# Kernel tuning notes

Hardware: AMD Instinct MI355X
Metric: run time of the kernel (lower is better)

Reference implementation:

```python
import jax, jax.numpy as jnp
import numpy as np

WS = (4, 4, 4)          # window size (d, h, w)
NUM_HEADS = 6
DIM = 192


def _relative_position_index(ws):
    # static int index, computed in numpy
    coords = np.stack(np.meshgrid(np.arange(ws[0]), np.arange(ws[1]), np.arange(ws[2]), indexing='ij'))  # (3, wd, wh, ww)
    coords = coords.reshape(3, -1)                      # (3, N)
    rel = coords[:, :, None] - coords[:, None, :]        # (3, N, N)
    rel = rel.transpose(1, 2, 0)                         # (N, N, 3)
    rel[:, :, 0] += ws[0] - 1
    rel[:, :, 1] += ws[1] - 1
    rel[:, :, 2] += ws[2] - 1
    rel[:, :, 0] *= (2 * ws[1] - 1) * (2 * ws[2] - 1)
    rel[:, :, 1] *= (2 * ws[2] - 1)
    return rel.sum(-1)                                   # (N, N)

_REL_IDX = _relative_position_index(WS)


def setup_inputs() -> dict:
    key = jax.random.key(0)
    ks = jax.random.split(key, 4)
    x = jax.random.normal(ks[0], (2, DIM, 46, 47, 48), dtype=jnp.float32)
    qkv_w = jax.random.normal(ks[1], (3 * DIM, DIM), dtype=jnp.float32) * 0.02
    qkv_b = jnp.zeros((3 * DIM,), dtype=jnp.float32)
    proj_w = jax.random.normal(ks[2], (DIM, DIM), dtype=jnp.float32) * 0.02
    proj_b = jnp.zeros((DIM,), dtype=jnp.float32)
    rpb_table = jax.random.normal(ks[3], ((2 * WS[0] - 1) * (2 * WS[1] - 1) * (2 * WS[2] - 1), NUM_HEADS), dtype=jnp.float32) * 0.02
    return {"x": x, "qkv_w": qkv_w, "qkv_b": qkv_b, "proj_w": proj_w, "proj_b": proj_b, "rpb_table": rpb_table}


def reference(x, qkv_w, qkv_b, proj_w, proj_b, rpb_table):
    B, C, D, H, W = x.shape
    wd, wh, ww = WS
    pd = (-D) % wd
    ph = (-H) % wh
    pw = (-W) % ww
    Dp, Hp, Wp = D + pd, H + ph, W + pw

    # BCDHW -> B,D,H,W,C then pad spatial dims (zero pad, same as F.pad on BCDHW)
    xc = jnp.transpose(x, (0, 2, 3, 4, 1))
    xc = jnp.pad(xc, ((0, 0), (0, pd), (0, ph), (0, pw), (0, 0)))

    # window partition -> (nW, N, C)
    Dw, Hw, Ww = Dp // wd, Hp // wh, Wp // ww
    xw = xc.reshape(B, Dw, wd, Hw, wh, Ww, ww, C)
    xw = jnp.transpose(xw, (0, 1, 3, 5, 2, 4, 6, 7)).reshape(-1, wd * wh * ww, C)
    N = wd * wh * ww

    # windowed MHA with relative position bias
    hd = C // NUM_HEADS
    qkv = xw @ qkv_w.T + qkv_b                               # (nW, N, 3C)
    qkv = qkv.reshape(-1, N, 3, NUM_HEADS, hd)
    q, k, v = (jnp.transpose(qkv[:, :, i], (0, 2, 1, 3)) for i in range(3))  # (nW, h, N, hd)
    scale = jnp.asarray(hd, x.dtype) ** -0.5
    attn = jnp.einsum('whnd,whmd->whnm', q * scale, k)       # (nW, h, N, N)
    bias = rpb_table[_REL_IDX.reshape(-1)].reshape(N, N, NUM_HEADS)
    bias = jnp.transpose(bias, (2, 0, 1))                    # (h, N, N)
    attn = jax.nn.softmax(attn + bias[None], axis=-1)
    out = jnp.einsum('whnm,whmd->whnd', attn, v)             # (nW, h, N, hd)
    out = jnp.transpose(out, (0, 2, 1, 3)).reshape(-1, N, C)
    out = out @ proj_w.T + proj_b

    # window reverse + crop, back to BCDHW
    xr = out.reshape(B, Dw, Hw, Ww, wd, wh, ww, C)
    xr = jnp.transpose(xr, (0, 1, 4, 2, 5, 3, 6, 7)).reshape(B, Dp, Hp, Wp, C)
    xr = jnp.transpose(xr, (0, 4, 1, 2, 3))[:, :, :D, :H, :W]
    return xr
```

## Files before the change

kernel.cpp:

```cpp
#include <hip/hip_runtime.h>

typedef __bf16 bf16x8 __attribute__((ext_vector_type(8)));
typedef __bf16 bf16x4 __attribute__((ext_vector_type(4)));
typedef float  f32x4  __attribute__((ext_vector_type(4)));

#define MFMA16(a, b, c) __builtin_amdgcn_mfma_f32_16x16x32_bf16((a), (b), (c), 0, 0, 0)

constexpr int Cdim = 192, NHd = 6;
constexpr int Dd = 46, Hh = 47, Wl = 48;
constexpr int HWst = Hh * Wl;
constexpr int NWIN_PER_B = 12 * 12 * 12;
constexpr int NBLK = 2 * NWIN_PER_B;
constexpr float SCALE = 0.17677669529663687f;

constexpr int WQ_ELEMS = 576 * 192;
constexpr int WP_ELEMS = 192 * 192;
constexpr size_t OFF_WQ   = 0;
constexpr size_t OFF_WP   = OFF_WQ + WQ_ELEMS;
constexpr size_t OFF_RPBT = OFF_WP + WP_ELEMS;
constexpr size_t WS_SMALL = (OFF_RPBT + 4128) * 2;

__device__ inline bf16x8 cvt8(const float* __restrict__ p) {
  f32x4 u0 = *(const f32x4*)p;
  f32x4 u1 = *(const f32x4*)(p + 4);
  bf16x8 r;
  r[0] = (__bf16)u0[0]; r[1] = (__bf16)u0[1]; r[2] = (__bf16)u0[2]; r[3] = (__bf16)u0[3];
  r[4] = (__bf16)u1[0]; r[5] = (__bf16)u1[1]; r[6] = (__bf16)u1[2]; r[7] = (__bf16)u1[3];
  return r;
}

__device__ inline bf16x4 pack4(f32x4 v) {
  bf16x4 r;
  r[0] = (__bf16)v[0]; r[1] = (__bf16)v[1]; r[2] = (__bf16)v[2]; r[3] = (__bf16)v[3];
  return r;
}

__device__ inline bf16x8 cat8(bf16x4 a, bf16x4 b) {
  bf16x8 r;
  r[0] = a[0]; r[1] = a[1]; r[2] = a[2]; r[3] = a[3];
  r[4] = b[0]; r[5] = b[1]; r[6] = b[2]; r[7] = b[3];
  return r;
}

__global__ __launch_bounds__(256) void convert_w_kernel(
    const float* __restrict__ qkv_w, const float* __restrict__ proj_w,
    const float* __restrict__ rpb,
    __bf16* __restrict__ wq, __bf16* __restrict__ wp, float* __restrict__ rpbt) {
  const int i = blockIdx.x * 256 + threadIdx.x;
  if (i < WQ_ELEMS) wq[i] = (__bf16)qkv_w[i];
  if (i < WP_ELEMS) wp[i] = (__bf16)proj_w[i];
  if (i < 343 * NHd) {
    const int h = i / 343, idx = i % 343;
    rpbt[h * 343 + idx] = rpb[idx * NHd + h];
  }
}

constexpr int XWA  = 204;
constexpr int QKLD = 36;
constexpr int VLD  = 68;
constexpr int BUFE = 2304;

__global__ __launch_bounds__(384, 4) void fused_kernel(
    const float* __restrict__ x, const float* __restrict__ qkv_b,
    const __bf16* __restrict__ wq, const __bf16* __restrict__ wp,
    const float* __restrict__ proj_b, const float* __restrict__ rpbt,
    float* __restrict__ out)
{
  __shared__ __bf16 xw[64 * XWA];
  __shared__ __bf16 bufs[6 * BUFE];
  const f32x4 fz = {0.f, 0.f, 0.f, 0.f};
  const int tid = threadIdx.x, lane = tid & 63, wv = tid >> 6;
  const int li = lane & 15, g = lane >> 4;
  const int hq = wv;
  const int bid = blockIdx.x;
  const int wid = (bid & 7) * (NBLK / 8) + (bid >> 3);
  const int b = wid / NWIN_PER_B, wr = wid % NWIN_PER_B;
  const int d0 = (wr / 144) * 4, h0 = ((wr / 12) % 12) * 4, w0 = (wr % 12) * 4;

  #pragma unroll
  for (int rep = 0; rep < 8; ++rep) {
    const int task = rep * 384 + tid;
    const int c = task % Cdim, ph = task / Cdim;
    const int dd = ph >> 2, hh = ph & 3;
    const int d = d0 + dd, hs = h0 + hh;
    f32x4 v = fz;
    if (d < Dd && hs < Hh)
      v = *(const f32x4*)(x + ((size_t)(b * Cdim + c) * Dd + d) * HWst + hs * Wl + w0);
    const int nb = (dd * 16 + hh * 4) * XWA + c;
    xw[nb]           = (__bf16)v[0];
    xw[nb + XWA]     = (__bf16)v[1];
    xw[nb + 2 * XWA] = (__bf16)v[2];
    xw[nb + 3 * XWA] = (__bf16)v[3];
  }
  __syncthreads();

  __bf16* buf = bufs + wv * BUFE;
  bf16x8 qfv[4], kfv[4], vav[2][2];

  {
    f32x4 acc[2][4];
    #pragma unroll
    for (int i = 0; i < 2; ++i)
      #pragma unroll
      for (int t = 0; t < 4; ++t) acc[i][t] = fz;
    #pragma unroll
    for (int kk = 0; kk < 6; ++kk) {
      const int k0 = kk * 32 + g * 8;
      bf16x8 xf[4];
      #pragma unroll
      for (int nt = 0; nt < 4; ++nt)
        xf[nt] = *(const bf16x8*)&xw[(nt * 16 + li) * XWA + k0];
      #pragma unroll
      for (int i = 0; i < 2; ++i) {
        bf16x8 wf = *(const bf16x8*)(wq + (size_t)((hq * 2 + i) * 16 + li) * Cdim + k0);
        #pragma unroll
        for (int nt = 0; nt < 4; ++nt)
          acc[i][nt] = MFMA16(wf, xf[nt], acc[i][nt]);
      }
    }
    #pragma unroll
    for (int i = 0; i < 2; ++i) {
      const f32x4 b4 = *(const f32x4*)(qkv_b + (hq * 2 + i) * 16 + g * 4);
      #pragma unroll
      for (int nt = 0; nt < 4; ++nt) {
        f32x4 val = (acc[i][nt] + b4) * SCALE;
        *(bf16x4*)&buf[(nt * 16 + li) * QKLD + i * 16 + g * 4] = pack4(val);
      }
    }
    #pragma unroll
    for (int t = 0; t < 4; ++t) {
      bf16x4 lo = *(const bf16x4*)&buf[(t * 16 + li) * QKLD + g * 8];
      bf16x4 hi = *(const bf16x4*)&buf[(t * 16 + li) * QKLD + g * 8 + 4];
      qfv[t] = cat8(lo, hi);
    }
  }

  {
    f32x4 acc[2][4];
    #pragma unroll
    for (int i = 0; i < 2; ++i)
      #pragma unroll
      for (int t = 0; t < 4; ++t) acc[i][t] = fz;
    #pragma unroll
    for (int kk = 0; kk < 6; ++kk) {
      const int k0 = kk * 32 + g * 8;
      bf16x8 xf[4];
      #pragma unroll
      for (int nt = 0; nt < 4; ++nt)
        xf[nt] = *(const bf16x8*)&xw[(nt * 16 + li) * XWA + k0];
      #pragma unroll
      for (int i = 0; i < 2; ++i) {
        bf16x8 wf = *(const bf16x8*)(wq + (size_t)(192 + (hq * 2 + i) * 16 + li) * Cdim + k0);
        #pragma unroll
        for (int nt = 0; nt < 4; ++nt)
          acc[i][nt] = MFMA16(wf, xf[nt], acc[i][nt]);
      }
    }
    #pragma unroll
    for (int i = 0; i < 2; ++i) {
      const f32x4 b4 = *(const f32x4*)(qkv_b + 192 + (hq * 2 + i) * 16 + g * 4);
      #pragma unroll
      for (int nt = 0; nt < 4; ++nt) {
        f32x4 val = acc[i][nt] + b4;
        *(bf16x4*)&buf[(nt * 16 + li) * QKLD + i * 16 + g * 4] = pack4(val);
      }
    }
    #pragma unroll
    for (int t = 0; t < 4; ++t) {
      bf16x4 lo = *(const bf16x4*)&buf[(t * 16 + li) * QKLD + g * 8];
      bf16x4 hi = *(const bf16x4*)&buf[(t * 16 + li) * QKLD + g * 8 + 4];
      kfv[t] = cat8(lo, hi);
    }
  }

  {
    f32x4 acc[2][4];
    #pragma unroll
    for (int i = 0; i < 2; ++i)
      #pragma unroll
      for (int t = 0; t < 4; ++t) acc[i][t] = fz;
    #pragma unroll
    for (int kk = 0; kk < 6; ++kk) {
      const int k0 = kk * 32 + g * 8;
      bf16x8 xf[4];
      #pragma unroll
      for (int rt = 0; rt < 4; ++rt)
        xf[rt] = *(const bf16x8*)&xw[(rt * 16 + li) * XWA + k0];
      #pragma unroll
      for (int i = 0; i < 2; ++i) {
        bf16x8 wf = *(const bf16x8*)(wq + (size_t)(384 + (hq * 2 + i) * 16 + li) * Cdim + k0);
        #pragma unroll
        for (int rt = 0; rt < 4; ++rt)
          acc[i][rt] = MFMA16(xf[rt], wf, acc[i][rt]);
      }
    }
    #pragma unroll
    for (int i = 0; i < 2; ++i) {
      const float bias = qkv_b[384 + (hq * 2 + i) * 16 + li];
      const f32x4 vb = {bias, bias, bias, bias};
      #pragma unroll
      for (int rt = 0; rt < 4; ++rt) {
        f32x4 val = acc[i][rt] + vb;
        *(bf16x4*)&buf[(i * 16 + li) * VLD + rt * 16 + g * 4] = pack4(val);
      }
    }
    #pragma unroll
    for (int rt = 0; rt < 2; ++rt)
      #pragma unroll
      for (int kk = 0; kk < 2; ++kk) {
        bf16x4 lo = *(const bf16x4*)&buf[(rt * 16 + li) * VLD + kk * 32 + g * 4];
        bf16x4 hi = *(const bf16x4*)&buf[(rt * 16 + li) * VLD + kk * 32 + 16 + g * 4];
        vav[rt][kk] = cat8(lo, hi);
      }
  }
  __syncthreads();

  __bf16* ao = xw;

  const int hbase = ((li >> 2) - g + 3) * 7 + (li & 3) + 3;
  float brow[7][4];
  {
    const float* rp = rpbt + hq * 343 + hbase - 3;
    #pragma unroll
    for (int dd = 0; dd < 7; ++dd)
      #pragma unroll
      for (int j = 0; j < 4; ++j)
        brow[dd][j] = rp[dd * 49 + j];
  }

  #pragma unroll
  for (int rb = 0; rb < 4; ++rb) {
    f32x4 s[4];
    #pragma unroll
    for (int ct = 0; ct < 4; ++ct) s[ct] = MFMA16(kfv[ct], qfv[rb], fz);

    float t[4][4];
    float rm = -3e38f;
    #pragma unroll
    for (int ct = 0; ct < 4; ++ct) {
      #pragma unroll
      for (int r = 0; r < 4; ++r) {
        const float tv = s[ct][r] + brow[rb - ct + 3][3 - r];
        t[ct][r] = tv;
        rm = fmaxf(rm, tv);
      }
    }
    rm = fmaxf(rm, __shfl_xor(rm, 16));
    rm = fmaxf(rm, __shfl_xor(rm, 32));
    float rs = 0.f;
    #pragma unroll
    for (int ct = 0; ct < 4; ++ct)
      #pragma unroll
      for (int r = 0; r < 4; ++r) {
        const float p = __expf(t[ct][r] - rm);
        t[ct][r] = p;
        rs += p;
      }
    rs += __shfl_xor(rs, 16);
    rs += __shfl_xor(rs, 32);
    const float rinv = 1.f / rs;

    bf16x4 ppk[4];
    #pragma unroll
    for (int ct = 0; ct < 4; ++ct) {
      f32x4 pv = {t[ct][0] * rinv, t[ct][1] * rinv, t[ct][2] * rinv, t[ct][3] * rinv};
      ppk[ct] = pack4(pv);
    }
    bf16x8 pa0 = cat8(ppk[0], ppk[1]);
    bf16x8 pa1 = cat8(ppk[2], ppk[3]);

    f32x4 o0 = fz, o1 = fz;
    o0 = MFMA16(vav[0][0], pa0, o0);
    o0 = MFMA16(vav[0][1], pa1, o0);
    o1 = MFMA16(vav[1][0], pa0, o1);
    o1 = MFMA16(vav[1][1], pa1, o1);
    *(bf16x4*)&ao[(rb * 16 + li) * XWA + hq * 32 + g * 4]      = pack4(o0);
    *(bf16x4*)&ao[(rb * 16 + li) * XWA + hq * 32 + 16 + g * 4] = pack4(o1);
  }
  __syncthreads();

  f32x4 pacc[2][4];
  #pragma unroll
  for (int i = 0; i < 2; ++i)
    #pragma unroll
    for (int rt = 0; rt < 4; ++rt) pacc[i][rt] = fz;
  #pragma unroll
  for (int kk = 0; kk < 6; ++kk) {
    const int k0 = kk * 32 + g * 8;
    bf16x8 af[4];
    #pragma unroll
    for (int rt = 0; rt < 4; ++rt)
      af[rt] = *(const bf16x8*)&ao[(rt * 16 + li) * XWA + k0];
    #pragma unroll
    for (int i = 0; i < 2; ++i) {
      const int c = (wv * 2 + i) * 16 + li;
      bf16x8 bf = *(const bf16x8*)(wp + (size_t)c * Cdim + k0);
      #pragma unroll
      for (int rt = 0; rt < 4; ++rt)
        pacc[i][rt] = MFMA16(af[rt], bf, pacc[i][rt]);
    }
  }
  #pragma unroll
  for (int i = 0; i < 2; ++i) {
    const int c = (wv * 2 + i) * 16 + li;
    const float pb = proj_b[c];
    #pragma unroll
    for (int rt = 0; rt < 4; ++rt) {
      const int d = d0 + rt, hs = h0 + g;
      if (d < Dd && hs < Hh) {
        f32x4 vv = {pacc[i][rt][0] + pb, pacc[i][rt][1] + pb,
                    pacc[i][rt][2] + pb, pacc[i][rt][3] + pb};
        *(f32x4*)(out + ((size_t)(b * Cdim + c) * Dd + d) * HWst + hs * Wl + w0) = vv;
      }
    }
  }
}

constexpr int XW_LD = 200, QK_LD = 36, VT_LD = 68, P_LDF = 68;
constexpr int XW_OFF  = 0;
constexpr int Q_OFF   = 25600;
constexpr int K_OFF   = Q_OFF + 27648;
constexpr int VT_OFF  = K_OFF + 27648;
constexpr int P_OFF   = VT_OFF + 26112;
constexpr int RPB_OFF = P_OFF + 26112;
constexpr int LDS_TOTAL = RPB_OFF + 8256;

__global__ __launch_bounds__(768, 3) void winattn_fused(
    const float* __restrict__ x, const float* __restrict__ qkv_w,
    const float* __restrict__ qkv_b, const float* __restrict__ proj_w,
    const float* __restrict__ proj_b, const float* __restrict__ rpb,
    float* __restrict__ out)
{
  extern __shared__ __align__(16) char smem[];
  __bf16* xw  = (__bf16*)(smem + XW_OFF);
  __bf16* qs  = (__bf16*)(smem + Q_OFF);
  __bf16* ks  = (__bf16*)(smem + K_OFF);
  __bf16* vt  = (__bf16*)(smem + VT_OFF);
  __bf16* pl  = (__bf16*)(smem + P_OFF);
  float*  rps = (float*)(smem + RPB_OFF);
  const f32x4 fz = {0.f, 0.f, 0.f, 0.f};
  const int tid = threadIdx.x, lane = tid & 63, wv = tid >> 6;
  const int hq = wv >> 1, half = wv & 1, li = lane & 15, g = lane >> 4;
  const int bid = blockIdx.x;
  const int wid = (bid & 7) * (NBLK / 8) + (bid >> 3);
  const int b = wid / NWIN_PER_B, wr = wid % NWIN_PER_B;
  const int d0 = (wr / 144) * 4, h0 = ((wr / 12) % 12) * 4, w0 = (wr % 12) * 4;
  for (int i = tid; i < 343 * NHd; i += 768) rps[i] = rpb[i];
  #pragma unroll
  for (int rep = 0; rep < 4; ++rep) {
    const int task = rep * 768 + tid;
    const int c = task % Cdim, ph = task / Cdim;
    const int dd = ph >> 2, hh2 = ph & 3;
    const int d = d0 + dd, hsp = h0 + hh2;
    f32x4 v = fz;
    if (d < Dd && hsp < Hh)
      v = *(const f32x4*)(x + ((size_t)(b * Cdim + c) * Dd + d) * HWst + hsp * Wl + w0);
    const int nb = (dd * 16 + hh2 * 4) * XW_LD + c;
    xw[nb] = (__bf16)v[0]; xw[nb + XW_LD] = (__bf16)v[1];
    xw[nb + 2 * XW_LD] = (__bf16)v[2]; xw[nb + 3 * XW_LD] = (__bf16)v[3];
  }
  __syncthreads();
  {
    f32x4 acc[6][2];
    #pragma unroll
    for (int it = 0; it < 6; ++it)
      #pragma unroll
      for (int rr = 0; rr < 2; ++rr) acc[it][rr] = fz;
    #pragma unroll
    for (int kk = 0; kk < 6; ++kk) {
      const int k0 = kk * 32 + g * 8;
      bf16x8 af[2];
      #pragma unroll
      for (int rr = 0; rr < 2; ++rr)
        af[rr] = *(const bf16x8*)&xw[((half * 2 + rr) * 16 + li) * XW_LD + k0];
      #pragma unroll
      for (int it = 0; it < 6; ++it) {
        const int T = (it >> 1) * 12 + hq * 2 + (it & 1);
        const int j = T * 16 + li;
        bf16x8 bf = cvt8(qkv_w + j * Cdim + k0);
        #pragma unroll
        for (int rr = 0; rr < 2; ++rr) acc[it][rr] = MFMA16(af[rr], bf, acc[it][rr]);
      }
    }
    #pragma unroll
    for (int it = 0; it < 6; ++it) {
      const int part = it >> 1, e16 = (it & 1) * 16;
      const int j0 = (part * 12 + hq * 2 + (it & 1)) * 16;
      const float qb = qkv_b[j0 + li];
      #pragma unroll
      for (int rr = 0; rr < 2; ++rr) {
        const int rb = half * 2 + rr;
        #pragma unroll
        for (int r = 0; r < 4; ++r) {
          const float val = acc[it][rr][r] + qb;
          const int n = rb * 16 + g * 4 + r;
          if (part == 0)      qs[(hq * 64 + n) * QK_LD + e16 + li] = (__bf16)val;
          else if (part == 1) ks[(hq * 64 + n) * QK_LD + e16 + li] = (__bf16)val;
          else                vt[(hq * 32 + e16 + li) * VT_LD + n] = (__bf16)val;
        }
      }
    }
  }
  __syncthreads();
  {
    __bf16* pw = pl + wv * 16 * P_LDF;
    #pragma unroll 1
    for (int rr = 0; rr < 2; ++rr) {
      const int rb = half * 2 + rr;
      bf16x8 aq = *(const bf16x8*)&qs[(hq * 64 + rb * 16 + li) * QK_LD + g * 8];
      f32x4 s[4];
      #pragma unroll
      for (int ct = 0; ct < 4; ++ct) {
        bf16x8 bk = *(const bf16x8*)&ks[(hq * 64 + ct * 16 + li) * QK_LD + g * 8];
        s[ct] = MFMA16(aq, bk, fz);
      }
      float t[4][4], rm[4] = {-3e38f, -3e38f, -3e38f, -3e38f};
      #pragma unroll
      for (int ct = 0; ct < 4; ++ct) {
        #pragma unroll
        for (int r = 0; r < 4; ++r) {
          const int idx = (rb - ct + 3) * 49 + (g - (li >> 2) + 3) * 7 + (r - (li & 3) + 3);
          const float tv = s[ct][r] * SCALE + rps[idx * NHd + hq];
          t[ct][r] = tv;
          rm[r] = fmaxf(rm[r], tv);
        }
      }
      #pragma unroll
      for (int r = 0; r < 4; ++r) {
        rm[r] = fmaxf(rm[r], __shfl_xor(rm[r], 1, 16));
        rm[r] = fmaxf(rm[r], __shfl_xor(rm[r], 2, 16));
        rm[r] = fmaxf(rm[r], __shfl_xor(rm[r], 4, 16));
        rm[r] = fmaxf(rm[r], __shfl_xor(rm[r], 8, 16));
      }
      float rs[4] = {0, 0, 0, 0};
      #pragma unroll
      for (int ct = 0; ct < 4; ++ct)
        #pragma unroll
        for (int r = 0; r < 4; ++r) {
          const float p = __expf(t[ct][r] - rm[r]);
          t[ct][r] = p; rs[r] += p;
        }
      #pragma unroll
      for (int r = 0; r < 4; ++r) {
        rs[r] += __shfl_xor(rs[r], 1, 16);
        rs[r] += __shfl_xor(rs[r], 2, 16);
        rs[r] += __shfl_xor(rs[r], 4, 16);
        rs[r] += __shfl_xor(rs[r], 8, 16);
      }
      #pragma unroll
      for (int ct = 0; ct < 4; ++ct)
        #pragma unroll
        for (int r = 0; r < 4; ++r)
          pw[(g * 4 + r) * P_LDF + ct * 16 + li] = (__bf16)t[ct][r];
      f32x4 o[2] = {fz, fz};
      #pragma unroll
      for (int kk = 0; kk < 2; ++kk) {
        bf16x8 ap = *(const bf16x8*)&pw[li * P_LDF + kk * 32 + g * 8];
        #pragma unroll
        for (int ct = 0; ct < 2; ++ct) {
          bf16x8 bv = *(const bf16x8*)&vt[(hq * 32 + ct * 16 + li) * VT_LD + kk * 32 + g * 8];
          o[ct] = MFMA16(ap, bv, o[ct]);
        }
      }
      float inv[4];
      #pragma unroll
      for (int r = 0; r < 4; ++r) inv[r] = 1.f / rs[r];
      #pragma unroll
      for (int ct = 0; ct < 2; ++ct)
        #pragma unroll
        for (int r = 0; r < 4; ++r)
          xw[(rb * 16 + g * 4 + r) * XW_LD + hq * 32 + ct * 16 + li] = (__bf16)(o[ct][r] * inv[r]);
    }
  }
  __syncthreads();
  {
    f32x4 acc[4];
    #pragma unroll
    for (int rt = 0; rt < 4; ++rt) acc[rt] = fz;
    const int c = wv * 16 + li;
    #pragma unroll
    for (int kk = 0; kk < 6; ++kk) {
      const int k0 = kk * 32 + g * 8;
      bf16x8 bf = cvt8(proj_w + c * Cdim + k0);
      #pragma unroll
      for (int rt = 0; rt < 4; ++rt) {
        bf16x8 af = *(const bf16x8*)&xw[(rt * 16 + li) * XW_LD + k0];
        acc[rt] = MFMA16(af, bf, acc[rt]);
      }
    }
    const float pb = proj_b[c];
    #pragma unroll
    for (int rt = 0; rt < 4; ++rt) {
      const int d = d0 + rt, hsp = h0 + g;
      if (d < Dd && hsp < Hh) {
        f32x4 vv = {acc[rt][0] + pb, acc[rt][1] + pb, acc[rt][2] + pb, acc[rt][3] + pb};
        *(f32x4*)(out + ((size_t)(b * Cdim + c) * Dd + d) * HWst + hsp * Wl + w0) = vv;
      }
    }
  }
}

extern "C" void kernel_launch(void* const* d_in, const int* in_sizes, int n_in,
                              void* d_out, int out_size, void* d_ws, size_t ws_size,
                              hipStream_t stream) {
  const float* x      = (const float*)d_in[0];
  const float* qkv_w  = (const float*)d_in[1];
  const float* qkv_b  = (const float*)d_in[2];
  const float* proj_w = (const float*)d_in[3];
  const float* proj_b = (const float*)d_in[4];
  const float* rpb    = (const float*)d_in[5];
  float* out = (float*)d_out;

  if (ws_size >= WS_SMALL) {
    __bf16* wsb  = (__bf16*)d_ws;
    __bf16* wq   = wsb + OFF_WQ;
    __bf16* wp   = wsb + OFF_WP;
    float*  rpbt = (float*)(wsb + OFF_RPBT);
    convert_w_kernel<<<(WQ_ELEMS + 255) / 256, 256, 0, stream>>>(qkv_w, proj_w, rpb, wq, wp, rpbt);
    fused_kernel<<<NBLK, 384, 0, stream>>>(x, qkv_b, wq, wp, proj_b, rpbt, out);
  } else {
    (void)hipFuncSetAttribute(reinterpret_cast<const void*>(&winattn_fused),
                              hipFuncAttributeMaxDynamicSharedMemorySize, LDS_TOTAL);
    winattn_fused<<<NBLK, 768, LDS_TOTAL, stream>>>(
        x, qkv_w, qkv_b, proj_w, proj_b, rpb, out);
  }
}
```

Baseline: 300.5 us.

## Process two adjacent windows per block with ping-pong LDS regions

Each block now handles two neighbouring windows along W instead of one, halving the grid. The relative-position bias rows are loaded once per block and reused for both windows. Two LDS regions swap roles, so the second window's input staging is issued right after the first window's projection, letting global loads overlap that epilogue. LDS per block grows (two 6*BUFE regions), which may reduce resident blocks per CU, and there is less block-level parallelism.

New measurement: 402.2 us. 1.34x slower.

```diff
diff --git a/kernel.cpp b/kernel.cpp
--- a/kernel.cpp
+++ b/kernel.cpp
@@ -11,6 +11,7 @@
 constexpr int HWst = Hh * Wl;
 constexpr int NWIN_PER_B = 12 * 12 * 12;
 constexpr int NBLK = 2 * NWIN_PER_B;
+constexpr int NPAIR = NBLK / 2;
 constexpr float SCALE = 0.17677669529663687f;
 
 constexpr int WQ_ELEMS = 576 * 192;
@@ -59,43 +60,40 @@
 constexpr int QKLD = 36;
 constexpr int VLD  = 68;
 constexpr int BUFE = 2304;
-
-__global__ __launch_bounds__(384, 4) void fused_kernel(
-    const float* __restrict__ x, const float* __restrict__ qkv_b,
-    const __bf16* __restrict__ wq, const __bf16* __restrict__ wp,
-    const float* __restrict__ proj_b, const float* __restrict__ rpbt,
-    float* __restrict__ out)
-{
-  __shared__ __bf16 xw[64 * XWA];
-  __shared__ __bf16 bufs[6 * BUFE];
+constexpr int REGE = 6 * BUFE;
+
+struct LaneCtx {
+  int tid, li, g, hq;
+  int b, d0, h0;
+};
+
+__device__ inline void stage_x(const float* __restrict__ x, __bf16* __restrict__ xw,
+                               const LaneCtx& L, int w0) {
   const f32x4 fz = {0.f, 0.f, 0.f, 0.f};
-  const int tid = threadIdx.x, lane = tid & 63, wv = tid >> 6;
-  const int li = lane & 15, g = lane >> 4;
-  const int hq = wv;
-  const int bid = blockIdx.x;
-  const int wid = (bid & 7) * (NBLK / 8) + (bid >> 3);
-  const int b = wid / NWIN_PER_B, wr = wid % NWIN_PER_B;
-  const int d0 = (wr / 144) * 4, h0 = ((wr / 12) % 12) * 4, w0 = (wr % 12) * 4;
-
   #pragma unroll
   for (int rep = 0; rep < 8; ++rep) {
-    const int task = rep * 384 + tid;
+    const int task = rep * 384 + L.tid;
     const int c = task % Cdim, ph = task / Cdim;
     const int dd = ph >> 2, hh = ph & 3;
-    const int d = d0 + dd, hs = h0 + hh;
+    const int d = L.d0 + dd, hs = L.h0 + hh;
     f32x4 v = fz;
     if (d < Dd && hs < Hh)
-      v = *(const f32x4*)(x + ((size_t)(b * Cdim + c) * Dd + d) * HWst + hs * Wl + w0);
+      v = *(const f32x4*)(x + ((size_t)(L.b * Cdim + c) * Dd + d) * HWst + hs * Wl + w0);
     const int nb = (dd * 16 + hh * 4) * XWA + c;
     xw[nb]           = (__bf16)v[0];
     xw[nb + XWA]     = (__bf16)v[1];
     xw[nb + 2 * XWA] = (__bf16)v[2];
     xw[nb + 3 * XWA] = (__bf16)v[3];
   }
-  __syncthreads();
-
-  __bf16* buf = bufs + wv * BUFE;
-  bf16x8 qfv[4], kfv[4], vav[2][2];
+}
+
+__device__ inline void gemm_qkv(const __bf16* __restrict__ xw, __bf16* __restrict__ bufreg,
+                                const float* __restrict__ qkv_b, const __bf16* __restrict__ wq,
+                                const LaneCtx& L,
+                                bf16x8 (&qfv)[4], bf16x8 (&kfv)[4], bf16x8 (&vav)[2][2]) {
+  const f32x4 fz = {0.f, 0.f, 0.f, 0.f};
+  const int li = L.li, g = L.g, hq = L.hq;
+  __bf16* buf = bufreg + hq * BUFE;
 
   {
     f32x4 acc[2][4];
@@ -134,7 +132,6 @@
       qfv[t] = cat8(lo, hi);
     }
   }
-
   {
     f32x4 acc[2][4];
     #pragma unroll
@@ -172,7 +169,6 @@
       kfv[t] = cat8(lo, hi);
     }
   }
-
   {
     f32x4 acc[2][4];
     #pragma unroll
@@ -213,21 +209,14 @@
         vav[rt][kk] = cat8(lo, hi);
       }
   }
-  __syncthreads();
-
-  __bf16* ao = xw;
-
-  const int hbase = ((li >> 2) - g + 3) * 7 + (li & 3) + 3;
-  float brow[7][4];
-  {
-    const float* rp = rpbt + hq * 343 + hbase - 3;
-    #pragma unroll
-    for (int dd = 0; dd < 7; ++dd)
-      #pragma unroll
-      for (int j = 0; j < 4; ++j)
-        brow[dd][j] = rp[dd * 49 + j];
-  }
-
+}
+
+__device__ inline void attn_phase(__bf16* __restrict__ ao, const LaneCtx& L,
+                                  const float (&brow)[7][4],
+                                  const bf16x8 (&qfv)[4], const bf16x8 (&kfv)[4],
+                                  const bf16x8 (&vav)[2][2]) {
+  const f32x4 fz = {0.f, 0.f, 0.f, 0.f};
+  const int li = L.li, g = L.g, hq = L.hq;
   #pragma unroll
   for (int rb = 0; rb < 4; ++rb) {
     f32x4 s[4];
@@ -277,8 +266,13 @@
     *(bf16x4*)&ao[(rb * 16 + li) * XWA + hq * 32 + g * 4]      = pack4(o0);
     *(bf16x4*)&ao[(rb * 16 + li) * XWA + hq * 32 + 16 + g * 4] = pack4(o1);
   }
-  __syncthreads();
-
+}
+
+__device__ inline void proj_phase(const __bf16* __restrict__ ao, const __bf16* __restrict__ wp,
+                                  const float* __restrict__ proj_b, const LaneCtx& L,
+                                  int w0, float* __restrict__ out) {
+  const f32x4 fz = {0.f, 0.f, 0.f, 0.f};
+  const int li = L.li, g = L.g, wv = L.hq;
   f32x4 pacc[2][4];
   #pragma unroll
   for (int i = 0; i < 2; ++i)
@@ -306,14 +300,64 @@
     const float pb = proj_b[c];
     #pragma unroll
     for (int rt = 0; rt < 4; ++rt) {
-      const int d = d0 + rt, hs = h0 + g;
+      const int d = L.d0 + rt, hs = L.h0 + g;
       if (d < Dd && hs < Hh) {
         f32x4 vv = {pacc[i][rt][0] + pb, pacc[i][rt][1] + pb,
                     pacc[i][rt][2] + pb, pacc[i][rt][3] + pb};
-        *(f32x4*)(out + ((size_t)(b * Cdim + c) * Dd + d) * HWst + hs * Wl + w0) = vv;
-      }
-    }
-  }
+        *(f32x4*)(out + ((size_t)(L.b * Cdim + c) * Dd + d) * HWst + hs * Wl + w0) = vv;
+      }
+    }
+  }
+}
+
+__global__ __launch_bounds__(384, 4) void fused_kernel(
+    const float* __restrict__ x, const float* __restrict__ qkv_b,
+    const __bf16* __restrict__ wq, const __bf16* __restrict__ wp,
+    const float* __restrict__ proj_b, const float* __restrict__ rpbt,
+    float* __restrict__ out)
+{
+  __shared__ __bf16 regA[REGE];
+  __shared__ __bf16 regB[REGE];
+  LaneCtx L;
+  L.tid = threadIdx.x;
+  const int lane = L.tid & 63;
+  L.li = lane & 15; L.g = lane >> 4; L.hq = L.tid >> 6;
+  const int bid = blockIdx.x;
+  const int pid = (bid & 7) * (NPAIR / 8) + (bid >> 3);
+  const int wid0 = pid * 2;
+  L.b = wid0 / NWIN_PER_B;
+  const int wr = wid0 % NWIN_PER_B;
+  L.d0 = (wr / 144) * 4; L.h0 = ((wr / 12) % 12) * 4;
+  const int w0 = (wr % 12) * 4;
+
+  const int hbase = ((L.li >> 2) - L.g + 3) * 7 + (L.li & 3) + 3;
+  float brow[7][4];
+  {
+    const float* rp = rpbt + L.hq * 343 + hbase - 3;
+    #pragma unroll
+    for (int dd = 0; dd < 7; ++dd)
+      #pragma unroll
+      for (int j = 0; j < 4; ++j)
+        brow[dd][j] = rp[dd * 49 + j];
+  }
+
+  bf16x8 qfv[4], kfv[4], vav[2][2];
+
+  stage_x(x, regA, L, w0);
+  __syncthreads();
+  gemm_qkv(regA, regB, qkv_b, wq, L, qfv, kfv, vav);
+  __syncthreads();
+  attn_phase(regA, L, brow, qfv, kfv, vav);
+  __syncthreads();
+  proj_phase(regA, wp, proj_b, L, w0, out);
+  stage_x(x, regB, L, w0 + 4);
+  __syncthreads();
+
+  gemm_qkv(regB, regA, qkv_b, wq, L, qfv, kfv, vav);
+  __syncthreads();
+  attn_phase(regB, L, brow, qfv, kfv, vav);
+  __syncthreads();
+  proj_phase(regB, wp, proj_b, L, w0 + 4, out);
 }
 
 constexpr int XW_LD = 200, QK_LD = 36, VT_LD = 68, P_LDF = 68;
@@ -517,7 +561,7 @@
     __bf16* wp   = wsb + OFF_WP;
     float*  rpbt = (float*)(wsb + OFF_RPBT);
     convert_w_kernel<<<(WQ_ELEMS + 255) / 256, 256, 0, stream>>>(qkv_w, proj_w, rpb, wq, wp, rpbt);
-    fused_kernel<<<NBLK, 384, 0, stream>>>(x, qkv_b, wq, wp, proj_b, rpbt, out);
+    fused_kernel<<<NPAIR, 384, 0, stream>>>(x, qkv_b, wq, wp, proj_b, rpbt, out);
   } else {
     (void)hipFuncSetAttribute(reinterpret_cast<const void*>(&winattn_fused),
                               hipFuncAttributeMaxDynamicSharedMemorySize, LDS_TOTAL);
```
